# Performance work log

Hardware: AMD Instinct MI355X
Metric: run time of the kernel (lower is better)

Reference implementation:

```python
import jax, jax.numpy as jnp
import numpy as np

B, A, OBS, NACT, H, D = 8192, 8, 128, 32, 256, 64  # batch, n_agents, obs_shape, n_actions, rnn_hidden_dim, attn_dim
N = B * A


def setup_inputs() -> dict:
    key = jax.random.key(0)
    ks = jax.random.split(key, 12)
    s = 0.02
    return {
        "o": jax.random.normal(ks[0], (N, OBS), dtype=jnp.float32),
        "o_next": jax.random.normal(ks[1], (N, OBS), dtype=jnp.float32),
        "h": jax.random.normal(ks[2], (N, H), dtype=jnp.float32),
        "actions": jax.random.uniform(ks[3], (N, A, NACT), dtype=jnp.float32),
        "wq_w": jax.random.normal(ks[4], (D, 2 * OBS), dtype=jnp.float32) * s,
        "wq_b": jnp.zeros((D,), dtype=jnp.float32),
        "wk_w": jax.random.normal(ks[5], (D, NACT), dtype=jnp.float32) * s,
        "wk_b": jnp.zeros((D,), dtype=jnp.float32),
        "wv1_w": jax.random.normal(ks[6], (D, H + NACT), dtype=jnp.float32) * s,
        "wv1_b": jnp.zeros((D,), dtype=jnp.float32),
        "wv2_w": jax.random.normal(ks[7], (NACT, D), dtype=jnp.float32) * s,
        "wv2_b": jnp.zeros((NACT,), dtype=jnp.float32),
    }


def reference(o, o_next, h, actions, wq_w, wq_b, wk_w, wk_b, wv1_w, wv1_b, wv2_w, wv2_b):
    n, a, nact = actions.shape           # [N, A, n_actions]
    d = wq_w.shape[0]                    # attn_dim
    hdim = h.shape[-1]
    b = n // a
    # query: [N, D]
    query = jnp.concatenate([o, o_next], axis=-1) @ wq_w.T + wq_b
    # key: [N, A, D]
    key = (actions.reshape(-1, nact) @ wk_w.T + wk_b).reshape(n, a, d)
    # value: repeat h per attended agent -> [B*A*A, H]
    h_rep = jnp.tile(h.reshape(b, a, hdim), (1, a, 1)).reshape(-1, hdim)
    inps_v = jnp.concatenate([h_rep, actions.reshape(-1, nact)], axis=-1)
    hid = jax.nn.relu(inps_v @ wv1_w.T + wv1_b)
    value = (hid @ wv2_w.T + wv2_b).reshape(n, a, nact)
    # attention scores with self-masked diagonal
    scale = 1.0 / (float(d) ** 0.5)
    scores = jnp.einsum('nd,nad->na', query * scale, key).reshape(b, a, a)
    eye = jnp.eye(a, dtype=bool)
    scores = jnp.where(eye[None, :, :], jnp.asarray(-1e9, scores.dtype), scores)
    attn = jax.nn.softmax(scores, axis=-1).reshape(n, a, 1)
    q = jnp.sum(value * attn, axis=1)    # [N, n_actions]
    return q
```

## Files before the change

kernel.cpp:

```cpp
#include <hip/hip_runtime.h>

typedef __attribute__((ext_vector_type(8))) short bf16x8;
typedef __attribute__((ext_vector_type(4))) float f32x4;

#define MFMA(A, B, C) __builtin_amdgcn_mfma_f32_16x16x32_bf16((A), (B), (C), 0, 0, 0)

#define OFF_TB    0
#define OFF_WT_H  128
#define OFF_WT_L  16512
#define OFF_WHV_H 32896
#define OFF_WHV_L 65664
#define OFF_WA_H  98432
#define OFF_WA_L  102528

#define SM_HV   0
#define SM_T    17408
#define SM_AT   26624
#define SM_SS   28672
#define SM_W2   38400
#define SM_TOT  46592

__device__ __forceinline__ unsigned short f2bf(float v) {
    unsigned u = __builtin_bit_cast(unsigned, v);
    return (unsigned short)((u + 0x7fffu + ((u >> 16) & 1u)) >> 16);
}
__device__ __forceinline__ float bf2f(unsigned short b) {
    return __builtin_bit_cast(float, ((unsigned)b) << 16);
}
__device__ __forceinline__ ushort2 splitf(float v) {
    unsigned short h = f2bf(v);
    unsigned short l = f2bf(v - bf2f(h));
    return make_ushort2(h, l);
}
__device__ __forceinline__ void split8(float4 a, float4 b, bf16x8& hi, bf16x8& lo) {
    float v[8] = {a.x, a.y, a.z, a.w, b.x, b.y, b.z, b.w};
    bf16x8 H, L;
#pragma unroll
    for (int i = 0; i < 8; ++i) {
        ushort2 s = splitf(v[i]);
        H[i] = (short)s.x;
        L[i] = (short)s.y;
    }
    hi = H; lo = L;
}

__global__ __launch_bounds__(256) void k_setup(const float* __restrict__ wq_w,
                                               const float* __restrict__ wq_b,
                                               const float* __restrict__ wk_w,
                                               const float* __restrict__ wv1,
                                               char* __restrict__ ws) {
    int gid = blockIdx.x * 256 + threadIdx.x;
    if (gid < 8192) {
        int k = gid >> 8, c = gid & 255;
        float acc = 0.f;
#pragma unroll 8
        for (int d = 0; d < 64; ++d) acc = fmaf(wk_w[d * 32 + k], wq_w[d * 256 + c], acc);
        ushort2 s = splitf(0.125f * acc);
        ((unsigned short*)(ws + OFF_WT_H))[gid] = s.x;
        ((unsigned short*)(ws + OFF_WT_L))[gid] = s.y;
    } else if (gid < 24576) {
        int i = gid - 8192;
        ushort2 s = splitf(wv1[(i >> 8) * 288 + (i & 255)]);
        ((unsigned short*)(ws + OFF_WHV_H))[i] = s.x;
        ((unsigned short*)(ws + OFF_WHV_L))[i] = s.y;
    } else if (gid < 26624) {
        int i = gid - 24576;
        ushort2 s = splitf(wv1[(i >> 5) * 288 + 256 + (i & 31)]);
        ((unsigned short*)(ws + OFF_WA_H))[i] = s.x;
        ((unsigned short*)(ws + OFF_WA_L))[i] = s.y;
    } else if (gid < 26656) {
        int k = gid - 26624;
        float b = 0.f;
#pragma unroll 8
        for (int d = 0; d < 64; ++d) b = fmaf(wk_w[d * 32 + k], wq_b[d], b);
        ((float*)(ws + OFF_TB))[k] = 0.125f * b;
    }
}

__global__ __launch_bounds__(256, 3) void fused(
    const float* __restrict__ o, const float* __restrict__ onx,
    const float* __restrict__ h, const float* __restrict__ act,
    const float* __restrict__ wv1b, const float* __restrict__ wv2,
    const float* __restrict__ wv2b, const char* __restrict__ ws,
    float* __restrict__ out)
{
    __shared__ __align__(16) char sm[SM_TOT];
    float* HV = (float*)(sm + SM_HV);
    float* T  = (float*)(sm + SM_T);
    float* AT = (float*)(sm + SM_AT);
    short* SS = (short*)(sm + SM_SS);
    float* W2 = (float*)(sm + SM_W2);

    const int tid  = threadIdx.x;
    const int lane = tid & 63;
    const int wid  = tid >> 6;
    const int l15  = lane & 15;
    const int quad = lane >> 4;
    const int n0   = blockIdx.x * 64;

    {
        const float4* wg = (const float4*)wv2;
        ((float4*)W2)[tid]       = wg[tid];
        ((float4*)W2)[tid + 256] = wg[tid + 256];
    }

    const f32x4 zv = {0.f, 0.f, 0.f, 0.f};
    f32x4 acc_hv[4] = {zv, zv, zv, zv};
    f32x4 acc_t[2]  = {zv, zv};

    const int myrow = n0 + wid * 16 + l15;

#pragma unroll
    for (int ch = 0; ch < 8; ++ch) {
        const float* src = (ch < 4)
            ? o   + (size_t)myrow * 128 + ch * 32 + quad * 8
            : onx + (size_t)myrow * 128 + (ch - 4) * 32 + quad * 8;
        float4 v0 = *(const float4*)src;
        float4 v1 = *(const float4*)(src + 4);
        bf16x8 Bh, Bl;
        split8(v0, v1, Bh, Bl);
#pragma unroll
        for (int mt = 0; mt < 2; ++mt) {
            int off = ((mt * 16 + l15) * 256 + ch * 32 + quad * 8) * 2;
            bf16x8 Ah = *(const bf16x8*)(ws + OFF_WT_H + off);
            bf16x8 Al = *(const bf16x8*)(ws + OFF_WT_L + off);
            acc_t[mt] = MFMA(Ah, Bh, acc_t[mt]);
            acc_t[mt] = MFMA(Ah, Bl, acc_t[mt]);
            acc_t[mt] = MFMA(Al, Bh, acc_t[mt]);
        }
    }
#pragma unroll
    for (int ch = 0; ch < 8; ++ch) {
        const float* src = h + (size_t)myrow * 256 + ch * 32 + quad * 8;
        float4 v0 = *(const float4*)src;
        float4 v1 = *(const float4*)(src + 4);
        bf16x8 Bh, Bl;
        split8(v0, v1, Bh, Bl);
#pragma unroll
        for (int mt = 0; mt < 4; ++mt) {
            int off = ((mt * 16 + l15) * 256 + ch * 32 + quad * 8) * 2;
            bf16x8 Ah = *(const bf16x8*)(ws + OFF_WHV_H + off);
            bf16x8 Al = *(const bf16x8*)(ws + OFF_WHV_L + off);
            acc_hv[mt] = MFMA(Ah, Bh, acc_hv[mt]);
            acc_hv[mt] = MFMA(Ah, Bl, acc_hv[mt]);
            acc_hv[mt] = MFMA(Al, Bh, acc_hv[mt]);
        }
    }
    {
        int erow = wid * 16 + l15;
        const float* tb = (const float*)(ws + OFF_TB);
#pragma unroll
        for (int mt = 0; mt < 4; ++mt) {
            int d0 = mt * 16 + quad * 4;
            float4 b = *(const float4*)&wv1b[d0];
            f32x4 a = acc_hv[mt];
            *(float4*)&HV[erow * 68 + d0] =
                make_float4(a[0] + b.x, a[1] + b.y, a[2] + b.z, a[3] + b.w);
        }
#pragma unroll
        for (int mt = 0; mt < 2; ++mt) {
            int k0 = mt * 16 + quad * 4;
            float4 b = *(const float4*)&tb[k0];
            f32x4 a = acc_t[mt];
            *(float4*)&T[erow * 36 + k0] =
                make_float4(a[0] + b.x, a[1] + b.y, a[2] + b.z, a[3] + b.w);
        }
    }
    __syncthreads();

    {
        float tr[32];
#pragma unroll
        for (int c4 = 0; c4 < 8; ++c4) {
            float4 v = *(const float4*)&T[lane * 36 + c4 * 4];
            tr[c4*4+0]=v.x; tr[c4*4+1]=v.y; tr[c4*4+2]=v.z; tr[c4*4+3]=v.w;
        }
        const float* arow = act + (size_t)(n0 + lane) * 256;
#pragma unroll
        for (int jj = 0; jj < 2; ++jj) {
            int j = wid * 2 + jj;
            float sc = 0.f;
#pragma unroll
            for (int c4 = 0; c4 < 8; ++c4) {
                float4 a = *(const float4*)(arow + j * 32 + c4 * 4);
                sc = fmaf(tr[c4*4+0], a.x, sc);
                sc = fmaf(tr[c4*4+1], a.y, sc);
                sc = fmaf(tr[c4*4+2], a.z, sc);
                sc = fmaf(tr[c4*4+3], a.w, sc);
            }
            AT[j * 64 + lane] = sc;
        }
    }
    bf16x8 WAh[4], WAl[4];
#pragma unroll
    for (int mt = 0; mt < 4; ++mt) {
        int off = ((mt * 16 + l15) * 32 + quad * 8) * 2;
        WAh[mt] = *(const bf16x8*)(ws + OFF_WA_H + off);
        WAl[mt] = *(const bf16x8*)(ws + OFF_WA_L + off);
    }
    __syncthreads();

    if (tid < 64) {
        int diag = tid & 7;
        float sc[8];
#pragma unroll
        for (int j = 0; j < 8; ++j) sc[j] = AT[j * 64 + tid];
        float mx = -1e30f;
#pragma unroll
        for (int j = 0; j < 8; ++j) if (j != diag) mx = fmaxf(mx, sc[j]);
        float e[8], sum = 0.f;
#pragma unroll
        for (int j = 0; j < 8; ++j) { e[j] = (j == diag) ? 0.f : __expf(sc[j] - mx); sum += e[j]; }
        float inv = 1.f / sum;
#pragma unroll
        for (int j = 0; j < 8; ++j) AT[j * 64 + tid] = e[j] * inv;
    }
    __syncthreads();

#pragma unroll
    for (int g = 0; g < 4; ++g) {
#pragma unroll
        for (int nt = 0; nt < 2; ++nt) {
            int njr = wid * 32 + nt * 16 + l15;
            int nb  = g * 16 + (njr >> 3);
            int j   = njr & 7;
            const float* ap = act + (size_t)(n0 + nb) * 256 + j * 32 + quad * 8;
            float4 v0 = *(const float4*)ap;
            float4 v1 = *(const float4*)(ap + 4);
            bf16x8 Bh, Bl;
            split8(v0, v1, Bh, Bl);
            f32x4 accB[4] = {zv, zv, zv, zv};
#pragma unroll
            for (int mt = 0; mt < 4; ++mt) {
                accB[mt] = MFMA(WAh[mt], Bh, accB[mt]);
                accB[mt] = MFMA(WAh[mt], Bl, accB[mt]);
                accB[mt] = MFMA(WAl[mt], Bh, accB[mt]);
            }
            int hrow = (nb & ~7) + j;
            float at = AT[j * 64 + nb];
#pragma unroll
            for (int mt = 0; mt < 4; ++mt) {
                int d0 = mt * 16 + quad * 4;
                float4 hv4 = *(const float4*)&HV[hrow * 68 + d0];
                float r0 = at * fmaxf(accB[mt][0] + hv4.x, 0.f);
                float r1 = at * fmaxf(accB[mt][1] + hv4.y, 0.f);
                float r2 = at * fmaxf(accB[mt][2] + hv4.z, 0.f);
                float r3 = at * fmaxf(accB[mt][3] + hv4.w, 0.f);
#pragma unroll
                for (int m = 1; m <= 4; m <<= 1) {
                    r0 += __shfl_xor(r0, m);
                    r1 += __shfl_xor(r1, m);
                    r2 += __shfl_xor(r2, m);
                    r3 += __shfl_xor(r3, m);
                }
                if (j == 0)
                    *(ushort4*)&SS[nb * 76 + d0] =
                        make_ushort4(f2bf(r0), f2bf(r1), f2bf(r2), f2bf(r3));
            }
        }
    }
    __syncthreads();

    {
        float s[64];
#pragma unroll
        for (int q = 0; q < 16; ++q) {
            ushort4 u = *(const ushort4*)&SS[lane * 76 + q * 4];
            s[q*4+0] = bf2f(u.x); s[q*4+1] = bf2f(u.y);
            s[q*4+2] = bf2f(u.z); s[q*4+3] = bf2f(u.w);
        }
        float qa[8];
#pragma unroll
        for (int e = 0; e < 8; ++e) qa[e] = wv2b[wid * 8 + e];
#pragma unroll
        for (int d4 = 0; d4 < 16; ++d4) {
#pragma unroll
            for (int e = 0; e < 8; ++e) {
                float4 w = *(const float4*)&W2[(wid * 8 + e) * 64 + d4 * 4];
                qa[e] = fmaf(w.x, s[d4*4+0], qa[e]);
                qa[e] = fmaf(w.y, s[d4*4+1], qa[e]);
                qa[e] = fmaf(w.z, s[d4*4+2], qa[e]);
                qa[e] = fmaf(w.w, s[d4*4+3], qa[e]);
            }
        }
        float* op = out + (size_t)(n0 + lane) * 32 + wid * 8;
        ((float4*)op)[0] = make_float4(qa[0], qa[1], qa[2], qa[3]);
        ((float4*)op)[1] = make_float4(qa[4], qa[5], qa[6], qa[7]);
    }
}

extern "C" void kernel_launch(void* const* d_in, const int* in_sizes, int n_in,
                              void* d_out, int out_size, void* d_ws, size_t ws_size,
                              hipStream_t stream) {
    const float* o     = (const float*)d_in[0];
    const float* onx   = (const float*)d_in[1];
    const float* h     = (const float*)d_in[2];
    const float* act   = (const float*)d_in[3];
    const float* wq_w  = (const float*)d_in[4];
    const float* wq_b  = (const float*)d_in[5];
    const float* wk_w  = (const float*)d_in[6];
    const float* wv1_w = (const float*)d_in[8];
    const float* wv1_b = (const float*)d_in[9];
    const float* wv2_w = (const float*)d_in[10];
    const float* wv2_b = (const float*)d_in[11];
    float* out = (float*)d_out;
    char* ws   = (char*)d_ws;

    k_setup<<<105, 256, 0, stream>>>(wq_w, wq_b, wk_w, wv1_w, ws);
    fused<<<1024, 256, 0, stream>>>(o, onx, h, act, wv1_b, wv2_w, wv2_b, ws, out);
}
```

Before: 277.3 us.

## Compute attention scores and softmax in registers, drop LDS stages and a barrier

Scores are now computed directly from the MFMA accumulator fragments, with cross-quad shuffle reductions, and each wave runs the softmax itself. This removes the T shared buffer, one __syncthreads and the single-wave softmax stage. Global loads of o/h/actions are batched ahead of the MFMA loops to expose memory-level parallelism, and W2 is read from global instead of being staged in LDS. The smaller LDS footprint and launch bounds raised to 4 blocks per SM aim for higher occupancy, at the risk of register pressure and spills from the larger prefetch arrays.

New measurement: 269.5 us. -2.8%, faster.

```diff
diff --git a/kernel.cpp b/kernel.cpp
--- a/kernel.cpp
+++ b/kernel.cpp
@@ -14,11 +14,9 @@
 #define OFF_WA_L  102528
 
 #define SM_HV   0
-#define SM_T    17408
-#define SM_AT   26624
-#define SM_SS   28672
-#define SM_W2   38400
-#define SM_TOT  46592
+#define SM_AT   17408
+#define SM_SS   19456
+#define SM_TOT  29184
 
 __device__ __forceinline__ unsigned short f2bf(float v) {
     unsigned u = __builtin_bit_cast(unsigned, v);
@@ -77,7 +75,7 @@
     }
 }
 
-__global__ __launch_bounds__(256, 3) void fused(
+__global__ __launch_bounds__(256, 4) void fused(
     const float* __restrict__ o, const float* __restrict__ onx,
     const float* __restrict__ h, const float* __restrict__ act,
     const float* __restrict__ wv1b, const float* __restrict__ wv2,
@@ -86,10 +84,8 @@
 {
     __shared__ __align__(16) char sm[SM_TOT];
     float* HV = (float*)(sm + SM_HV);
-    float* T  = (float*)(sm + SM_T);
     float* AT = (float*)(sm + SM_AT);
     short* SS = (short*)(sm + SM_SS);
-    float* W2 = (float*)(sm + SM_W2);
 
     const int tid  = threadIdx.x;
     const int lane = tid & 63;
@@ -98,27 +94,25 @@
     const int quad = lane >> 4;
     const int n0   = blockIdx.x * 64;
 
-    {
-        const float4* wg = (const float4*)wv2;
-        ((float4*)W2)[tid]       = wg[tid];
-        ((float4*)W2)[tid + 256] = wg[tid + 256];
-    }
-
     const f32x4 zv = {0.f, 0.f, 0.f, 0.f};
     f32x4 acc_hv[4] = {zv, zv, zv, zv};
     f32x4 acc_t[2]  = {zv, zv};
 
     const int myrow = n0 + wid * 16 + l15;
 
+    float4 xa[8], xb[8];
 #pragma unroll
     for (int ch = 0; ch < 8; ++ch) {
         const float* src = (ch < 4)
             ? o   + (size_t)myrow * 128 + ch * 32 + quad * 8
             : onx + (size_t)myrow * 128 + (ch - 4) * 32 + quad * 8;
-        float4 v0 = *(const float4*)src;
-        float4 v1 = *(const float4*)(src + 4);
+        xa[ch] = ((const float4*)src)[0];
+        xb[ch] = ((const float4*)src)[1];
+    }
+#pragma unroll
+    for (int ch = 0; ch < 8; ++ch) {
         bf16x8 Bh, Bl;
-        split8(v0, v1, Bh, Bl);
+        split8(xa[ch], xb[ch], Bh, Bl);
 #pragma unroll
         for (int mt = 0; mt < 2; ++mt) {
             int off = ((mt * 16 + l15) * 256 + ch * 32 + quad * 8) * 2;
@@ -132,10 +126,13 @@
 #pragma unroll
     for (int ch = 0; ch < 8; ++ch) {
         const float* src = h + (size_t)myrow * 256 + ch * 32 + quad * 8;
-        float4 v0 = *(const float4*)src;
-        float4 v1 = *(const float4*)(src + 4);
+        xa[ch] = ((const float4*)src)[0];
+        xb[ch] = ((const float4*)src)[1];
+    }
+#pragma unroll
+    for (int ch = 0; ch < 8; ++ch) {
         bf16x8 Bh, Bl;
-        split8(v0, v1, Bh, Bl);
+        split8(xa[ch], xb[ch], Bh, Bl);
 #pragma unroll
         for (int mt = 0; mt < 4; ++mt) {
             int off = ((mt * 16 + l15) * 256 + ch * 32 + quad * 8) * 2;
@@ -146,9 +143,17 @@
             acc_hv[mt] = MFMA(Al, Bh, acc_hv[mt]);
         }
     }
+
+    const float* arow = act + (size_t)myrow * 256;
+    float4 av0[8], av1[8];
+#pragma unroll
+    for (int j = 0; j < 8; ++j) {
+        av0[j] = *(const float4*)(arow + j * 32 + quad * 4);
+        av1[j] = *(const float4*)(arow + j * 32 + 16 + quad * 4);
+    }
+
     {
         int erow = wid * 16 + l15;
-        const float* tb = (const float*)(ws + OFF_TB);
 #pragma unroll
         for (int mt = 0; mt < 4; ++mt) {
             int d0 = mt * 16 + quad * 4;
@@ -157,40 +162,58 @@
             *(float4*)&HV[erow * 68 + d0] =
                 make_float4(a[0] + b.x, a[1] + b.y, a[2] + b.z, a[3] + b.w);
         }
+    }
+
+    {
+        float t8[8];
+        const float* tb = (const float*)(ws + OFF_TB);
 #pragma unroll
         for (int mt = 0; mt < 2; ++mt) {
-            int k0 = mt * 16 + quad * 4;
-            float4 b = *(const float4*)&tb[k0];
-            f32x4 a = acc_t[mt];
-            *(float4*)&T[erow * 36 + k0] =
-                make_float4(a[0] + b.x, a[1] + b.y, a[2] + b.z, a[3] + b.w);
-        }
-    }
-    __syncthreads();
-
-    {
-        float tr[32];
-#pragma unroll
-        for (int c4 = 0; c4 < 8; ++c4) {
-            float4 v = *(const float4*)&T[lane * 36 + c4 * 4];
-            tr[c4*4+0]=v.x; tr[c4*4+1]=v.y; tr[c4*4+2]=v.z; tr[c4*4+3]=v.w;
-        }
-        const float* arow = act + (size_t)(n0 + lane) * 256;
-#pragma unroll
-        for (int jj = 0; jj < 2; ++jj) {
-            int j = wid * 2 + jj;
-            float sc = 0.f;
-#pragma unroll
-            for (int c4 = 0; c4 < 8; ++c4) {
-                float4 a = *(const float4*)(arow + j * 32 + c4 * 4);
-                sc = fmaf(tr[c4*4+0], a.x, sc);
-                sc = fmaf(tr[c4*4+1], a.y, sc);
-                sc = fmaf(tr[c4*4+2], a.z, sc);
-                sc = fmaf(tr[c4*4+3], a.w, sc);
-            }
-            AT[j * 64 + lane] = sc;
-        }
-    }
+            float4 b = *(const float4*)&tb[mt * 16 + quad * 4];
+            t8[mt * 4 + 0] = acc_t[mt][0] + b.x;
+            t8[mt * 4 + 1] = acc_t[mt][1] + b.y;
+            t8[mt * 4 + 2] = acc_t[mt][2] + b.z;
+            t8[mt * 4 + 3] = acc_t[mt][3] + b.w;
+        }
+        float sc[8];
+#pragma unroll
+        for (int j = 0; j < 8; ++j) {
+            float s = 0.f;
+            s = fmaf(t8[0], av0[j].x, s);
+            s = fmaf(t8[1], av0[j].y, s);
+            s = fmaf(t8[2], av0[j].z, s);
+            s = fmaf(t8[3], av0[j].w, s);
+            s = fmaf(t8[4], av1[j].x, s);
+            s = fmaf(t8[5], av1[j].y, s);
+            s = fmaf(t8[6], av1[j].z, s);
+            s = fmaf(t8[7], av1[j].w, s);
+            sc[j] = s;
+        }
+#pragma unroll
+        for (int j = 0; j < 8; ++j) {
+            sc[j] += __shfl_xor(sc[j], 16);
+            sc[j] += __shfl_xor(sc[j], 32);
+        }
+        const int diag = l15 & 7;
+        float mx = -1e30f;
+#pragma unroll
+        for (int j = 0; j < 8; ++j) if (j != diag) mx = fmaxf(mx, sc[j]);
+        float ex[8], sum = 0.f;
+#pragma unroll
+        for (int j = 0; j < 8; ++j) {
+            ex[j] = (j == diag) ? 0.f : __expf(sc[j] - mx);
+            sum += ex[j];
+        }
+        float inv = 1.f / sum;
+        if (quad == 0) {
+            int row = wid * 16 + l15;
+            *(float4*)&AT[row * 8] =
+                make_float4(ex[0] * inv, ex[1] * inv, ex[2] * inv, ex[3] * inv);
+            *(float4*)&AT[row * 8 + 4] =
+                make_float4(ex[4] * inv, ex[5] * inv, ex[6] * inv, ex[7] * inv);
+        }
+    }
+
     bf16x8 WAh[4], WAl[4];
 #pragma unroll
     for (int mt = 0; mt < 4; ++mt) {
@@ -200,35 +223,27 @@
     }
     __syncthreads();
 
-    if (tid < 64) {
-        int diag = tid & 7;
-        float sc[8];
-#pragma unroll
-        for (int j = 0; j < 8; ++j) sc[j] = AT[j * 64 + tid];
-        float mx = -1e30f;
-#pragma unroll
-        for (int j = 0; j < 8; ++j) if (j != diag) mx = fmaxf(mx, sc[j]);
-        float e[8], sum = 0.f;
-#pragma unroll
-        for (int j = 0; j < 8; ++j) { e[j] = (j == diag) ? 0.f : __expf(sc[j] - mx); sum += e[j]; }
-        float inv = 1.f / sum;
-#pragma unroll
-        for (int j = 0; j < 8; ++j) AT[j * 64 + tid] = e[j] * inv;
-    }
-    __syncthreads();
-
-#pragma unroll
-    for (int g = 0; g < 4; ++g) {
-#pragma unroll
-        for (int nt = 0; nt < 2; ++nt) {
+#pragma unroll
+    for (int half = 0; half < 2; ++half) {
+        float4 bv0[4], bv1[4];
+        int nbs[4], js[4];
+#pragma unroll
+        for (int ii = 0; ii < 4; ++ii) {
+            int g   = half * 2 + (ii >> 1);
+            int nt  = ii & 1;
             int njr = wid * 32 + nt * 16 + l15;
             int nb  = g * 16 + (njr >> 3);
             int j   = njr & 7;
             const float* ap = act + (size_t)(n0 + nb) * 256 + j * 32 + quad * 8;
-            float4 v0 = *(const float4*)ap;
-            float4 v1 = *(const float4*)(ap + 4);
+            bv0[ii] = ((const float4*)ap)[0];
+            bv1[ii] = ((const float4*)ap)[1];
+            nbs[ii] = nb; js[ii] = j;
+        }
+#pragma unroll
+        for (int ii = 0; ii < 4; ++ii) {
+            int nb = nbs[ii], j = js[ii];
             bf16x8 Bh, Bl;
-            split8(v0, v1, Bh, Bl);
+            split8(bv0[ii], bv1[ii], Bh, Bl);
             f32x4 accB[4] = {zv, zv, zv, zv};
 #pragma unroll
             for (int mt = 0; mt < 4; ++mt) {
@@ -237,7 +252,7 @@
                 accB[mt] = MFMA(WAl[mt], Bh, accB[mt]);
             }
             int hrow = (nb & ~7) + j;
-            float at = AT[j * 64 + nb];
+            float at = AT[nb * 8 + j];
 #pragma unroll
             for (int mt = 0; mt < 4; ++mt) {
                 int d0 = mt * 16 + quad * 4;
@@ -262,28 +277,29 @@
     __syncthreads();
 
     {
+        int row = wid * 16 + l15;
         float s[64];
 #pragma unroll
         for (int q = 0; q < 16; ++q) {
-            ushort4 u = *(const ushort4*)&SS[lane * 76 + q * 4];
+            ushort4 u = *(const ushort4*)&SS[row * 76 + q * 4];
             s[q*4+0] = bf2f(u.x); s[q*4+1] = bf2f(u.y);
             s[q*4+2] = bf2f(u.z); s[q*4+3] = bf2f(u.w);
         }
         float qa[8];
 #pragma unroll
-        for (int e = 0; e < 8; ++e) qa[e] = wv2b[wid * 8 + e];
+        for (int e0 = 0; e0 < 8; ++e0) qa[e0] = wv2b[quad * 8 + e0];
 #pragma unroll
         for (int d4 = 0; d4 < 16; ++d4) {
 #pragma unroll
-            for (int e = 0; e < 8; ++e) {
-                float4 w = *(const float4*)&W2[(wid * 8 + e) * 64 + d4 * 4];
-                qa[e] = fmaf(w.x, s[d4*4+0], qa[e]);
-                qa[e] = fmaf(w.y, s[d4*4+1], qa[e]);
-                qa[e] = fmaf(w.z, s[d4*4+2], qa[e]);
-                qa[e] = fmaf(w.w, s[d4*4+3], qa[e]);
+            for (int e0 = 0; e0 < 8; ++e0) {
+                float4 w = *(const float4*)&wv2[(quad * 8 + e0) * 64 + d4 * 4];
+                qa[e0] = fmaf(w.x, s[d4*4+0], qa[e0]);
+                qa[e0] = fmaf(w.y, s[d4*4+1], qa[e0]);
+                qa[e0] = fmaf(w.z, s[d4*4+2], qa[e0]);
+                qa[e0] = fmaf(w.w, s[d4*4+3], qa[e0]);
             }
         }
-        float* op = out + (size_t)(n0 + lane) * 32 + wid * 8;
+        float* op = out + (size_t)(n0 + row) * 32 + quad * 8;
         ((float4*)op)[0] = make_float4(qa[0], qa[1], qa[2], qa[3]);
         ((float4*)op)[1] = make_float4(qa[4], qa[5], qa[6], qa[7]);
     }
```
